# Kernel optimization log

Hardware: AMD Instinct MI355X
Metric: run time of the kernel (lower is better)

## Reference

```python
import jax, jax.numpy as jnp
import numpy as np
from jax import lax

DT = 0.001          # integration step
SCALE = 0.2         # hopf_input_scale
NUM_STEPS = 5       # Euler sub-steps per sequence position
MU = 1.0            # Hopf limit-cycle radius^2


def hopf_layer(h, omega):
    """Hopf oscillator bank driven by h: [B, T, U]; omega: [U] (rad/s).
    For each sequence position, run NUM_STEPS Euler steps of
      dx = (mu - (x^2+y^2)) x - omega*y + scale*u
      dy = (mu - (x^2+y^2)) y + omega*x
    carrying (x, y) state across positions. Returns per-position states
    (z_real, z_imag), each [B, T, U]."""

    def per_timestep(state, u):  # u: [B, U]
        def euler(c, _):
            x, y = c
            r2 = x * x + y * y
            nx = x + DT * ((MU - r2) * x - omega * y + SCALE * u)
            ny = y + DT * ((MU - r2) * y + omega * x)
            return (nx, ny), None
        state, _ = lax.scan(euler, state, None, length=NUM_STEPS)
        return state, state

    B, T, U = h.shape
    z0 = (jnp.zeros((B, U), h.dtype), jnp.zeros((B, U), h.dtype))
    _, (xs, ys) = lax.scan(per_timestep, z0, jnp.swapaxes(h, 0, 1))  # [T,B,U]
    return jnp.swapaxes(xs, 0, 1), jnp.swapaxes(ys, 0, 1)


def setup_inputs() -> dict:
    key = jax.random.key(0)
    ks = jax.random.split(key, 12)
    B, T = 128, 1024
    V, E, U, P, C = 50000, 100, 100, 20, 2
    two_pi = 2.0 * np.pi
    return {
        "x": jax.random.randint(ks[0], (B, T), 0, V),
        "emb": jax.random.normal(ks[1], (V, E), jnp.float32) * 0.05,
        "omega1": jax.random.uniform(ks[2], (U,), jnp.float32, two_pi * 1.0, two_pi * 15.0),
        "omega2": jax.random.uniform(ks[3], (U,), jnp.float32, two_pi * 1.0, two_pi * 15.0),
        "w1": jax.random.normal(ks[4], (2 * U, U), jnp.float32) * 0.07,
        "b1": jnp.zeros((U,), jnp.float32),
        "w2": jax.random.normal(ks[5], (2 * U, U), jnp.float32) * 0.07,
        "b2": jnp.zeros((U,), jnp.float32),
        "wp": jax.random.normal(ks[6], (U, P), jnp.float32) * 0.1,
        "bp": jnp.zeros((P,), jnp.float32),
        "wh": jax.random.normal(ks[7], (P, C), jnp.float32) * 0.2,
        "bh": jnp.zeros((C,), jnp.float32),
    }


def reference(x, emb, omega1, omega2, w1, b1, w2, b2, wp, bp, wh, bh):
    h0 = emb[x]                                   # [B, T, E]
    z1r, z1i = hopf_layer(h0, omega1)             # [B, T, U] each
    h1 = jax.nn.relu(jnp.concatenate([z1r, z1i], axis=2) @ w1 + b1)
    z2r, z2i = hopf_layer(h1, omega2)
    h2 = jax.nn.relu(jnp.concatenate([z2r, z2i], axis=2) @ w2 + b2)
    last = h2[:, -1, :]                           # many-to-one: last timestep
    h3 = jnp.tanh(last @ wp + bp)                 # [B, P]
    return h3 @ wh + bh                           # [B, C]
```

## Files before the change

kernel.cpp:

```cpp
#include <hip/hip_runtime.h>
#include <cmath>

namespace {
constexpr int T = 1024, BATCH = 128, U = 100, E = 100, P = 20, C = 2;
constexpr int TC = 64, NC = 16;
constexpr float DT = 0.001f, SCALE = 0.2f, MU = 1.0f;
constexpr float DTS = DT * SCALE;

constexpr uint32_t WROW = 464u, ZROW = 464u, EROW = 128u, HROW = 128u;
constexpr uint32_t WLB = 0u;
constexpr uint32_t ZBB = 46400u, ZBUF = 29696u;
constexpr uint32_t EBB = 105792u, EBUF = 12800u;
constexpr uint32_t HBB = 131392u, HBUF = 12800u;
constexpr uint32_t XAB = 156992u;
constexpr uint32_t ARENA = 161088u;

typedef _Float16 f16x8 __attribute__((ext_vector_type(8)));
typedef _Float16 f16x4 __attribute__((ext_vector_type(4)));
typedef float f32x16 __attribute__((ext_vector_type(16)));
typedef float f32x2 __attribute__((ext_vector_type(2)));
typedef _Float16 h2_t __attribute__((ext_vector_type(2)));

__device__ __forceinline__ void eul5p(f32x2& v, float dom, float ax) {
    constexpr float c0 = 1.0f + DT * MU;
    const f32x2 dd = {-dom, dom};
    const f32x2 aa = {ax, 0.f};
#pragma unroll
    for (int s = 0; s < 5; ++s) {
        float r2 = fmaf(v[1], v[1], v[0] * v[0]);
        float sc = fmaf(-DT, r2, c0);
        f32x2 vyx = __builtin_shufflevector(v, v, 1, 0);
        f32x2 w = __builtin_elementwise_fma(vyx, dd, aa);
        f32x2 scv = {sc, sc};
        v = __builtin_elementwise_fma(v, scv, w);
    }
}

__device__ __forceinline__ h2_t cvt2h(float a, float b) {
    auto r = __builtin_amdgcn_cvt_pkrtz(a, b);
    return __builtin_bit_cast(h2_t, r);
}

__launch_bounds__(512, 1)
__global__ void donn_kernel(const int* __restrict__ xg,
                            const float* __restrict__ emb,
                            const float* __restrict__ omega1,
                            const float* __restrict__ omega2,
                            const float* __restrict__ w1,
                            const float* __restrict__ b1,
                            const float* __restrict__ w2,
                            const float* __restrict__ b2,
                            const float* __restrict__ wp,
                            const float* __restrict__ bp,
                            const float* __restrict__ wh,
                            const float* __restrict__ bh,
                            float* __restrict__ out)
{
    const int b = blockIdx.x;
    const int tid = threadIdx.x;

    __shared__ __align__(16) char smem[ARENA];
    int* xa = (int*)(smem + XAB);

    f32x2 v1 = {0.f, 0.f}, v2 = {0.f, 0.f};
    float dom1 = 0.f, dom2 = 0.f;
    int jc = 0, j2c = 0;
    bool act1 = false;
    int lane = 0, mh = 0, np = 0, mw = 0;
    float b1r[2] = {0.f, 0.f};
    uint32_t brow[2] = {0u, 0u};

    if (tid < 128) {
        jc = (tid < U) ? tid : (U - 1);
        act1 = tid < U;
        dom1 = DT * omega1[jc];
    } else if (tid < 256) {
        const int j2 = tid - 128;
        j2c = (j2 < U) ? j2 : (U - 1);
        dom2 = DT * omega2[j2c];
    } else {
        mw = (tid >> 6) - 4;
        lane = tid & 63;
        mh = mw >> 1;
        np = mw & 1;
#pragma unroll
        for (int nt = 0; nt < 2; ++nt) {
            int j = np * 64 + nt * 32 + (lane & 31);
            int jj = (j < U) ? j : (U - 1);
            b1r[nt] = b1[jj];
            brow[nt] = WLB + (uint32_t)jj * WROW + 16u * (uint32_t)(lane >> 5);
        }
    }

    for (int i = tid; i < T; i += 512) xa[i] = xg[b * T + i];
    for (int idx = tid; idx < 200 * 100; idx += 512) {
        int k = idx / 100, j = idx - 100 * k;
        int kp = (k < U) ? (2 * k) : (2 * (k - U) + 1);
        *(_Float16*)(smem + WLB + (uint32_t)j * WROW + 2u * (uint32_t)kp) = (_Float16)w1[k * U + j];
    }
    for (int idx = tid; idx < 100 * 16; idx += 512) {
        int row = idx >> 4, wd = idx & 15;
        *(float*)(smem + WLB + (uint32_t)row * WROW + 400u + 4u * (uint32_t)wd) = 0.f;
    }
    for (int idx = tid; idx < 128 * 16; idx += 512) {
        int zr = idx >> 4, wd = idx & 15;
        uint32_t base = ZBB + (uint32_t)(zr >> 6) * ZBUF + (uint32_t)(zr & 63) * ZROW;
        *(float*)(smem + base + 400u + 4u * (uint32_t)wd) = 0.f;
    }
    __syncthreads();
    for (int idx = tid; idx < 100 * TC; idx += 512) {
        int j = idx >> 6, t = idx & 63;
        int tok = xa[t];
        uint32_t off = EBB + (uint32_t)j * EROW
                     + (uint32_t)(((((t >> 3) ^ (j & 7))) << 4) + 2 * (t & 7));
        *(_Float16*)(smem + off) = (_Float16)emb[tok * E + j];
    }
    __syncthreads();

    if (tid < 256) __builtin_amdgcn_s_setprio(1);

    for (int p = 0; p <= NC + 1; ++p) {
        if (tid < 128) {
            if (p < NC) {
                const uint32_t q = (uint32_t)(p & 1);
                const char* ebase = smem + EBB + q * EBUF + (uint32_t)jc * EROW;
                char* zbase = smem + ZBB + q * ZBUF + 4u * (uint32_t)tid;
                const int s = jc & 7;
                f16x8 e0 = *(const f16x8*)(ebase + ((0 ^ s) << 4));
                f16x8 e1 = *(const f16x8*)(ebase + ((1 ^ s) << 4));
                for (int gg = 0; gg < 8; ++gg) {
                    f16x8 e2 = e1;
                    if (gg + 2 < 8) e2 = *(const f16x8*)(ebase + (((gg + 2) ^ s) << 4));
                    char* zt = zbase + (uint32_t)(8 * gg) * ZROW;
#pragma unroll
                    for (int i = 0; i < 8; ++i) {
                        eul5p(v1, dom1, DTS * (float)e0[i]);
                        if (act1) {
                            h2_t zz = cvt2h(v1[0], v1[1]);
                            *(h2_t*)(zt + (uint32_t)i * ZROW) = zz;
                        }
                    }
                    e0 = e1; e1 = e2;
                }
            }
        } else if (tid < 256) {
            if (p >= 2) {
                const uint32_t q = (uint32_t)(p & 1);
                const char* hbase = smem + HBB + q * HBUF + (uint32_t)j2c * HROW;
                const int s = j2c & 7;
                f16x8 e0 = *(const f16x8*)(hbase + ((0 ^ s) << 4));
                f16x8 e1 = *(const f16x8*)(hbase + ((1 ^ s) << 4));
                for (int gg = 0; gg < 8; ++gg) {
                    f16x8 e2 = e1;
                    if (gg + 2 < 8) e2 = *(const f16x8*)(hbase + (((gg + 2) ^ s) << 4));
#pragma unroll
                    for (int i = 0; i < 8; ++i)
                        eul5p(v2, dom2, DTS * (float)e0[i]);
                    e0 = e1; e1 = e2;
                }
            }
        } else {
            float er[25];
            const bool edo = (p + 1 < NC);
            if (edo) {
                int tok = xa[(p + 1) * TC + lane];
                const float* ep = emb + (size_t)tok * E;
#pragma unroll
                for (int i = 0; i < 25; ++i) er[i] = ep[mw * 25 + i];
            }
            if (p >= 1 && p <= NC) {
                const uint32_t qm = (uint32_t)((p - 1) & 1);
                const char* zb = smem + ZBB + qm * ZBUF;
                const uint32_t arow = (uint32_t)(mh * 32 + (lane & 31)) * ZROW
                                      + 16u * (uint32_t)(lane >> 5);
                f32x16 acc0 = (f32x16)0.f, acc1 = (f32x16)0.f;
#pragma unroll
                for (int ks = 0; ks < 14; ++ks) {
                    f16x8 af = *(const f16x8*)(zb + arow + 32u * ks);
                    f16x8 bf0 = *(const f16x8*)(smem + brow[0] + 32u * ks);
                    acc0 = __builtin_amdgcn_mfma_f32_32x32x16_f16(af, bf0, acc0, 0, 0, 0);
                    f16x8 bf1 = *(const f16x8*)(smem + brow[1] + 32u * ks);
                    acc1 = __builtin_amdgcn_mfma_f32_32x32x16_f16(af, bf1, acc1, 0, 0, 0);
                }
                char* hb = smem + HBB + qm * HBUF;
#pragma unroll
                for (int nt = 0; nt < 2; ++nt) {
                    const int j = np * 64 + nt * 32 + (lane & 31);
                    if (j < U) {
#pragma unroll
                        for (int g = 0; g < 4; ++g) {
                            const int tb = mh * 32 + 8 * g + 4 * (lane >> 5);
                            f16x4 hv;
#pragma unroll
                            for (int r = 0; r < 4; ++r) {
                                float vv = (nt == 0) ? acc0[4 * g + r] : acc1[4 * g + r];
                                hv[r] = (_Float16)fmaxf(vv + b1r[nt], 0.f);
                            }
                            uint32_t off = (uint32_t)j * HROW
                                + (uint32_t)(((((tb >> 3) ^ (j & 7))) << 4) + ((2 * tb) & 15));
                            *(f16x4*)(hb + off) = hv;
                        }
                    }
                }
            }
            if (edo) {
                const uint32_t qe = (uint32_t)((p + 1) & 1);
                char* eb = smem + EBB + qe * EBUF;
#pragma unroll
                for (int i = 0; i < 25; ++i) {
                    int jrow = mw * 25 + i;
                    uint32_t off = (uint32_t)jrow * EROW
                        + (uint32_t)(((((lane >> 3) ^ (jrow & 7))) << 4) + 2 * (lane & 7));
                    *(_Float16*)(eb + off) = (_Float16)er[i];
                }
            }
        }
        __syncthreads();
    }

    if (tid < 256) __builtin_amdgcn_s_setprio(0);

    float* zf2 = (float*)(smem + EBB);
    float* pb  = (float*)(smem + EBB + 832u);
    float* h2s = (float*)(smem + EBB + 1664u);
    float* h3s = (float*)(smem + EBB + 2080u);

    if (tid >= 128 && tid < 256) {
        const int j = tid - 128;
        if (j < U) { zf2[j] = v2[0]; zf2[104 + j] = v2[1]; }
    }
    __syncthreads();

    if (tid >= 256 && tid < 456) {
        const int e = tid - 256;
        const int h = e / 100, jq = e - 100 * (e / 100);
        float acc2 = 0.f;
#pragma unroll 4
        for (int kk = 0; kk < 100; ++kk)
            acc2 = fmaf(zf2[104 * h + kk], w2[(100 * h + kk) * U + jq], acc2);
        pb[104 * h + jq] = acc2;
    }
    __syncthreads();

    if (tid < U) h2s[tid] = fmaxf(pb[tid] + pb[104 + tid] + b2[tid], 0.f);
    __syncthreads();

    if (tid < P) {
        float acc = bp[tid];
#pragma unroll 4
        for (int j = 0; j < U; ++j) acc = fmaf(h2s[j], wp[j * P + tid], acc);
        h3s[tid] = tanhf(acc);
    }
    __syncthreads();

    if (tid < C) {
        float acc = bh[tid];
#pragma unroll
        for (int pp = 0; pp < P; ++pp) acc = fmaf(h3s[pp], wh[pp * C + tid], acc);
        out[b * C + tid] = acc;
    }
}
}

extern "C" void kernel_launch(void* const* d_in, const int* in_sizes, int n_in,
                              void* d_out, int out_size, void* d_ws, size_t ws_size,
                              hipStream_t stream) {
    const int* xi        = (const int*)d_in[0];
    const float* emb     = (const float*)d_in[1];
    const float* omega1  = (const float*)d_in[2];
    const float* omega2  = (const float*)d_in[3];
    const float* w1      = (const float*)d_in[4];
    const float* b1      = (const float*)d_in[5];
    const float* w2      = (const float*)d_in[6];
    const float* b2      = (const float*)d_in[7];
    const float* wp      = (const float*)d_in[8];
    const float* bp      = (const float*)d_in[9];
    const float* wh      = (const float*)d_in[10];
    const float* bh      = (const float*)d_in[11];
    float* out           = (float*)d_out;

    hipLaunchKernelGGL(donn_kernel, dim3(BATCH), dim3(512), 0, stream,
                       xi, emb, omega1, omega2, w1, b1, w2, b2, wp, bp, wh, bh, out);
}
```

Measured before the change: 119.7 us.

## Store embedding buffer token-major and coalesce embedding gathers

The embedding staging buffer changes from feature-major swizzled rows to token-major rows with a 208-byte pitch. The prefetch warps now fetch whole embedding rows with lanes spread across features, using readlane to broadcast each token id, so global reads are coalesced instead of strided per lane. The layer-1 oscillator threads now read one fp16 scalar per timestep from LDS rather than 8-wide vectors, trading fewer global transactions for more, narrower LDS reads.

New measurement: 141.6 us. 18.3% more time.

```diff
diff --git a/kernel.cpp b/kernel.cpp
--- a/kernel.cpp
+++ b/kernel.cpp
@@ -7,13 +7,13 @@
 constexpr float DT = 0.001f, SCALE = 0.2f, MU = 1.0f;
 constexpr float DTS = DT * SCALE;
 
-constexpr uint32_t WROW = 464u, ZROW = 464u, EROW = 128u, HROW = 128u;
+constexpr uint32_t WROW = 464u, ZROW = 464u, EROW = 208u, HROW = 128u;
 constexpr uint32_t WLB = 0u;
 constexpr uint32_t ZBB = 46400u, ZBUF = 29696u;
-constexpr uint32_t EBB = 105792u, EBUF = 12800u;
-constexpr uint32_t HBB = 131392u, HBUF = 12800u;
-constexpr uint32_t XAB = 156992u;
-constexpr uint32_t ARENA = 161088u;
+constexpr uint32_t EBB = 105792u, EBUF = 13312u;
+constexpr uint32_t HBB = 132416u, HBUF = 12800u;
+constexpr uint32_t XAB = 158016u;
+constexpr uint32_t ARENA = 162112u;
 
 typedef _Float16 f16x8 __attribute__((ext_vector_type(8)));
 typedef _Float16 f16x4 __attribute__((ext_vector_type(4)));
@@ -108,12 +108,11 @@
         *(float*)(smem + base + 400u + 4u * (uint32_t)wd) = 0.f;
     }
     __syncthreads();
-    for (int idx = tid; idx < 100 * TC; idx += 512) {
-        int j = idx >> 6, t = idx & 63;
+    for (int idx = tid; idx < TC * E; idx += 512) {
+        int t = idx / 100, j = idx - 100 * t;
         int tok = xa[t];
-        uint32_t off = EBB + (uint32_t)j * EROW
-                     + (uint32_t)(((((t >> 3) ^ (j & 7))) << 4) + 2 * (t & 7));
-        *(_Float16*)(smem + off) = (_Float16)emb[tok * E + j];
+        *(_Float16*)(smem + EBB + (uint32_t)t * EROW + 2u * (uint32_t)j) =
+            (_Float16)emb[tok * E + j];
     }
     __syncthreads();
 
@@ -123,24 +122,19 @@
         if (tid < 128) {
             if (p < NC) {
                 const uint32_t q = (uint32_t)(p & 1);
-                const char* ebase = smem + EBB + q * EBUF + (uint32_t)jc * EROW;
+                const char* eb = smem + EBB + q * EBUF + 2u * (uint32_t)jc;
                 char* zbase = smem + ZBB + q * ZBUF + 4u * (uint32_t)tid;
-                const int s = jc & 7;
-                f16x8 e0 = *(const f16x8*)(ebase + ((0 ^ s) << 4));
-                f16x8 e1 = *(const f16x8*)(ebase + ((1 ^ s) << 4));
-                for (int gg = 0; gg < 8; ++gg) {
-                    f16x8 e2 = e1;
-                    if (gg + 2 < 8) e2 = *(const f16x8*)(ebase + (((gg + 2) ^ s) << 4));
-                    char* zt = zbase + (uint32_t)(8 * gg) * ZROW;
-#pragma unroll
-                    for (int i = 0; i < 8; ++i) {
-                        eul5p(v1, dom1, DTS * (float)e0[i]);
-                        if (act1) {
-                            h2_t zz = cvt2h(v1[0], v1[1]);
-                            *(h2_t*)(zt + (uint32_t)i * ZROW) = zz;
-                        }
-                    }
-                    e0 = e1; e1 = e2;
+                float u0 = DTS * (float)(*(const _Float16*)(eb + 0u * EROW));
+                float u1 = DTS * (float)(*(const _Float16*)(eb + 1u * EROW));
+#pragma unroll 4
+                for (int t = 0; t < TC; ++t) {
+                    float u2 = 0.f;
+                    if (t + 2 < TC)
+                        u2 = DTS * (float)(*(const _Float16*)(eb + (uint32_t)(t + 2) * EROW));
+                    eul5p(v1, dom1, u0);
+                    if (act1)
+                        *(h2_t*)(zbase + (uint32_t)t * ZROW) = cvt2h(v1[0], v1[1]);
+                    u0 = u1; u1 = u2;
                 }
             }
         } else if (tid < 256) {
@@ -160,13 +154,18 @@
                 }
             }
         } else {
-            float er[25];
+            float rv0[16], rv1[16];
             const bool edo = (p + 1 < NC);
+            int tokv = 0;
             if (edo) {
-                int tok = xa[(p + 1) * TC + lane];
-                const float* ep = emb + (size_t)tok * E;
-#pragma unroll
-                for (int i = 0; i < 25; ++i) er[i] = ep[mw * 25 + i];
+                tokv = xa[(p + 1) * TC + mw * 16 + (lane & 15)];
+#pragma unroll
+                for (int r = 0; r < 16; ++r) {
+                    int tok = __builtin_amdgcn_readlane(tokv, r);
+                    const float* ep = emb + (size_t)tok * E;
+                    rv0[r] = ep[lane];
+                    rv1[r] = ep[64 + ((lane < 36) ? lane : 35)];
+                }
             }
             if (p >= 1 && p <= NC) {
                 const uint32_t qm = (uint32_t)((p - 1) & 1);
@@ -207,11 +206,11 @@
                 const uint32_t qe = (uint32_t)((p + 1) & 1);
                 char* eb = smem + EBB + qe * EBUF;
 #pragma unroll
-                for (int i = 0; i < 25; ++i) {
-                    int jrow = mw * 25 + i;
-                    uint32_t off = (uint32_t)jrow * EROW
-                        + (uint32_t)(((((lane >> 3) ^ (jrow & 7))) << 4) + 2 * (lane & 7));
-                    *(_Float16*)(eb + off) = (_Float16)er[i];
+                for (int r = 0; r < 16; ++r) {
+                    char* rowp = eb + (uint32_t)(mw * 16 + r) * EROW;
+                    *(_Float16*)(rowp + 2u * (uint32_t)lane) = (_Float16)rv0[r];
+                    if (lane < 36)
+                        *(_Float16*)(rowp + 2u * (uint32_t)(64 + lane)) = (_Float16)rv1[r];
                 }
             }
         }
```
